# Kernel tuning notes

Measured on AMD Instinct MI355X. Metric: run time of the kernel, lower is better.

The kernel has to match this reference:

```python
import jax, jax.numpy as jnp
import numpy as np

B, T, C, H, E, L = 4, 1024, 768, 12, 4, 2
DH = C // H


def setup_inputs() -> dict:
    key = jax.random.key(0)
    ks = jax.random.split(key, 10)
    s = 0.02  # init scale; keeps unscaled-attention logits sane (source has no 1/sqrt(d))
    w = lambda k, shape: (jax.random.normal(k, shape, jnp.float32) * s)
    z = lambda shape: jnp.zeros(shape, jnp.float32)
    return dict(
        x=jax.random.normal(ks[0], (B, T, C), jnp.float32),
        gate_W=w(ks[1], (C, E)), gate_b=z((E,)),
        Wq=w(ks[2], (E, L, C, C)), bq=z((E, L, C)),
        Wk=w(ks[3], (E, L, C, C)), bk=z((E, L, C)),
        Wv=w(ks[4], (E, L, C, C)), bv=z((E, L, C)),
        Wo=w(ks[5], (E, L, C, C)), bo=z((E, L, C)),
        ln_g=jnp.ones((E, L, C), jnp.float32), ln_b=z((E, L, C)),
        Wfc=w(ks[6], (E, L, C, 4 * C)), bfc=z((E, L, 4 * C)),
        Wpr=w(ks[7], (E, L, 4 * C, C)), bpr=z((E, L, C)),
    )


def _attn(x, Wq, bq, Wk, bk, Wv, bv, Wo, bo):
    # FlashAttention3 blockwise loop == exact full softmax(Q K^T) V, NO scaling, NO mask
    q = (x @ Wq + bq).reshape(B, T, H, DH)
    k = (x @ Wk + bk).reshape(B, T, H, DH)
    v = (x @ Wv + bv).reshape(B, T, H, DH)
    s = jnp.einsum('bqhd,bkhd->bhqk', q, k)
    p = jax.nn.softmax(s, axis=-1)
    o = jnp.einsum('bhqk,bkhd->bqhd', p, v).reshape(B, T, C)
    return o @ Wo + bo


def _ln(x, g, b, eps=1e-5):
    m = x.mean(-1, keepdims=True)
    v = ((x - m) ** 2).mean(-1, keepdims=True)
    return (x - m) * jax.lax.rsqrt(v + eps) * g + b


def _expert(x, Wq, bq, Wk, bk, Wv, bv, Wo, bo, ln_g, ln_b, Wfc, bfc, Wpr, bpr):
    # Sequential(attn, layernorm, mlp) x L — no residuals, dropout=0 (eval)
    for l in range(L):
        x = _attn(x, Wq[l], bq[l], Wk[l], bk[l], Wv[l], bv[l], Wo[l], bo[l])
        x = _ln(x, ln_g[l], ln_b[l])
        h = jax.nn.gelu(x @ Wfc[l] + bfc[l], approximate=True)  # tanh GELU
        x = h @ Wpr[l] + bpr[l]
    return x


def reference(x, gate_W, gate_b, Wq, bq, Wk, bk, Wv, bv, Wo, bo,
              ln_g, ln_b, Wfc, bfc, Wpr, bpr):
    gate_probs = jax.nn.softmax(x @ gate_W + gate_b, axis=-1)  # [B,T,E]
    expert_fn = jax.vmap(_expert, in_axes=(None,) + (0,) * 14)
    eo = expert_fn(x, Wq, bq, Wk, bk, Wv, bv, Wo, bo, ln_g, ln_b, Wfc, bfc, Wpr, bpr)  # [E,B,T,C]
    return jnp.einsum('bte,ebtc->btc', gate_probs, eo)
```

## Files before the change

### kernel.cpp

```cpp
#include <hip/hip_runtime.h>

#define B_ 4
#define T_ 1024
#define C_ 768
#define H_ 12
#define E_ 4
#define L_ 2
#define DH_ 64
#define M_ (B_*T_)
#define QKVS_ (3*C_)
#define LOG2E_ 1.4426950408889634f

typedef __attribute__((ext_vector_type(8))) short bf16x8;
typedef __attribute__((ext_vector_type(4))) float f32x4;

__device__ __forceinline__ unsigned short f2bf(float f) {
  unsigned int u = __float_as_uint(f);
  unsigned int r = (u + 0x7FFFu + ((u >> 16) & 1u)) >> 16;
  return (unsigned short)r;
}
__device__ __forceinline__ float bf2f(unsigned short s) {
  return __uint_as_float(((unsigned int)s) << 16);
}
__device__ __forceinline__ unsigned int cvt_pk_bf16(float lo, float hi) {
  unsigned int r;
  asm("v_cvt_pk_bf16_f32 %0, %1, %2" : "=v"(r) : "v"(lo), "v"(hi));
  return r;
}

typedef __attribute__((address_space(1))) unsigned int gu32;
typedef __attribute__((address_space(3))) unsigned int lu32;
__device__ __forceinline__ void gld_lds16(const void* g, void* l) {
  __builtin_amdgcn_global_load_lds((gu32*)g, (lu32*)l, 16, 0, 0);
}

__device__ __forceinline__ float gelu_fast(float x) {
  float u = 0.7978845608028654f * x * (1.0f + 0.044715f * x * x);
  float d = 1.0f + exp2f(-2.8853900817779268f * u);
  return x * __builtin_amdgcn_rcpf(d);
}

template <int ACT>
__global__ __launch_bounds__(512, 2) void gemm256(
    const unsigned short* __restrict__ A, const unsigned short* __restrict__ Bt,
    const float* __restrict__ bias, unsigned short* __restrict__ D,
    int M, int N, int K, long long sA, long long sB, long long sBias, long long sD,
    float bscale)
{
  __shared__ unsigned short shA[4][256*32];
  __shared__ unsigned short shB[4][256*32];
  const int tid = threadIdx.x;
  const int lane = tid & 63, wid = tid >> 6;
  const int l15 = lane & 15, lhi = lane >> 4;
  const int wm = wid >> 2, wn = wid & 3;

  const int gx = gridDim.x, gxy = gx * gridDim.y;
  const int nwg = gxy * gridDim.z;
  int flat = blockIdx.z*gxy + blockIdx.y*gx + blockIdx.x;
  flat = (flat & 7) * (nwg >> 3) + (flat >> 3);
  const int g = flat / gxy;
  const int rem = flat - g*gxy;
  const int by = rem / gx, bx = rem - by*gx;
  const int m0 = by * 256, n0 = bx * 256;

  const unsigned short* Ab = A + (size_t)g * sA;
  const unsigned short* Bb = Bt + (size_t)g * sB;
  const float* biasb = bias + (size_t)g * sBias;
  unsigned short* Db = D + (size_t)g * sD;

  f32x4 acc[8][4] = {};

  const int l15h = l15 >> 1;
  const int s8 = (((((l15 & 1) << 2) | lhi) ^ (l15h & 7)) << 3);
  const int arp = wm*64;
  const int brp = wn*32;

  auto stageA = [&](int slot, int kh) {
    const int kb = kh << 5;
    #pragma unroll
    for (int iss = 0; iss < 2; ++iss) {
      const int c = tid + iss*512;
      const int q = c >> 3, pp = (c & 7) ^ (q & 7);
      gld_lds16(Ab + (size_t)(m0 + (q << 1) + (pp >> 2))*K + kb + ((pp & 3) << 3),
                &shA[slot][c*8]);
    }
  };
  auto stageB = [&](int slot, int kh) {
    const int kb = kh << 5;
    #pragma unroll
    for (int iss = 0; iss < 2; ++iss) {
      const int c = tid + iss*512;
      const int q = c >> 3, pp = (c & 7) ^ (q & 7);
      gld_lds16(Bb + (size_t)(n0 + (q << 1) + (pp >> 2))*K + kb + ((pp & 3) << 3),
                &shB[slot][c*8]);
    }
  };

  auto phase = [&](int slot, int mh, int stSel, int stSlot, int stKh, int vmN) {
    bf16x8 afr[4], bfr[4];
    #pragma unroll
    for (int i = 0; i < 4; ++i)
      afr[i] = *(const bf16x8*)&shA[slot][(arp + mh*32 + i*8 + l15h)*64 + s8];
    #pragma unroll
    for (int nf = 0; nf < 4; ++nf)
      bfr[nf] = *(const bf16x8*)&shB[slot][(brp + nf*8 + l15h)*64 + s8];
    if (stSel == 1) stageA(stSlot, stKh);
    else if (stSel == 2) stageB(stSlot, stKh);
    if (vmN == 4) asm volatile("s_waitcnt vmcnt(4)" ::: "memory");
    else if (vmN == 0) asm volatile("s_waitcnt vmcnt(0)" ::: "memory");
    __builtin_amdgcn_s_barrier();
    __builtin_amdgcn_s_setprio(1);
    #pragma unroll
    for (int i = 0; i < 4; ++i)
      #pragma unroll
      for (int nf = 0; nf < 4; ++nf)
        acc[mh*4+i][nf] = __builtin_amdgcn_mfma_f32_16x16x32_bf16(
            afr[i], bfr[nf], acc[mh*4+i][nf], 0, 0, 0);
    __builtin_amdgcn_s_setprio(0);
    __builtin_amdgcn_s_barrier();
  };

  const int nkt = K >> 6;
  const int nkh = nkt << 1;

  stageA(0, 0); stageB(0, 0);
  stageA(1, 1); stageB(1, 1);
  stageA(2, 2); stageB(2, 2);
  asm volatile("s_waitcnt vmcnt(4)" ::: "memory");
  __builtin_amdgcn_s_barrier();

  for (int k = 0; k < nkt; ++k) {
    const int s0 = (2*k) & 3, s1 = s0 + 1;
    const int m3 = 2*k + 3, m4 = 2*k + 4;
    const bool f3 = m3 < nkh, f4 = m4 < nkh;
    phase(s0, 0, f3 ? 1 : 0, m3 & 3, m3, -1);
    phase(s0, 1, f3 ? 2 : 0, m3 & 3, m3, -1);
    phase(s1, 0, f4 ? 1 : 0, m4 & 3, m4, -1);
    phase(s1, 1, f4 ? 2 : 0, m4 & 3, m4, f4 ? 4 : (f3 ? 0 : -1));
  }

  unsigned short* cbuf = (unsigned short*)&shA[0][0];
  const int lr = tid >> 4, ckk = tid & 15;
  const int growb = m0 + ((lr >> 4) ? 128 : 0) + (lr & 15);
  #pragma unroll
  for (int mf = 0; mf < 8; ++mf) {
    __builtin_amdgcn_s_barrier();
    #pragma unroll
    for (int nf = 0; nf < 4; ++nf) {
      const int col = wn*64 + nf*16 + l15;
      const float bv = bscale * biasb[n0 + col];
      #pragma unroll
      for (int r = 0; r < 4; ++r) {
        float v = acc[mf][nf][r] + bv;
        if (ACT == 1) v = gelu_fast(v);
        cbuf[(wm*16 + lhi*4 + r)*264 + col] = f2bf(v);
      }
    }
    __builtin_amdgcn_s_barrier();
    const size_t growN = (size_t)(growb + mf*16) * N + n0;
    #pragma unroll
    for (int cc2 = 0; cc2 < 2; ++cc2) {
      const int c = ckk + cc2*16;
      uint4 v = *(const uint4*)&cbuf[lr*264 + c*8];
      *(uint4*)&Db[growN + c*8] = v;
    }
  }
}

__global__ __launch_bounds__(256) void flash_attn(
    const unsigned short* __restrict__ qkv, const unsigned short* __restrict__ vt,
    unsigned short* __restrict__ o)
{
  __shared__ unsigned short shK[2][64*64];
  __shared__ unsigned short shV[2][64*64];
  __shared__ unsigned short shP[4][16*64];
  const int tid = threadIdx.x;
  const int wid = tid >> 6, lane = tid & 63;
  const int l15 = lane & 15, lhi = lane >> 4;
  const int qt = blockIdx.x, h = blockIdx.y, eb = blockIdx.z;

  const unsigned short* qrow = qkv + ((size_t)eb*T_ + qt*64 + wid*16 + l15) * QKVS_ + h*DH_;
  bf16x8 aq0 = *(const bf16x8*)(qrow + lhi*8);
  bf16x8 aq1 = *(const bf16x8*)(qrow + 32 + lhi*8);

  f32x4 oacc[4] = {};
  float lpart = 0.f;

  const int krow = tid >> 3;
  const int swzsrc = (((tid & 7) ^ (krow & 7)) << 3);
  const unsigned short* kbase = qkv + (size_t)eb*T_*QKVS_ + C_ + h*DH_;
  const unsigned short* vbase = vt + ((size_t)eb*H_ + h)*DH_*T_;

  auto stage = [&](int buf, int kt) {
    #pragma unroll
    for (int p = 0; p < 2; ++p) {
      gld_lds16(kbase + (size_t)(kt*64 + krow + p*32)*QKVS_ + swzsrc,
                &shK[buf][(p*256 + wid*64)*8]);
      gld_lds16(vbase + (size_t)(krow + p*32)*T_ + kt*64 + swzsrc,
                &shV[buf][(p*256 + wid*64)*8]);
    }
  };

  stage(0, 0);
  __syncthreads();
  int cur = 0;
  const int swzr = l15 & 7;
  const int c0 = (lhi ^ swzr) << 3;
  const int c1 = ((4 + lhi) ^ swzr) << 3;
  const int pwbase = l15*64 + ((lhi & 1) << 2);
  const int pwh = lhi >> 1;

  for (int kt = 0; kt < T_/64; ++kt) {
    if (kt + 1 < T_/64) stage(cur ^ 1, kt + 1);

    f32x4 s[4];
    #pragma unroll
    for (int kb = 0; kb < 4; ++kb) {
      const int row = (kb*16 + l15)*64;
      bf16x8 bk0 = *(const bf16x8*)&shK[cur][row + c0];
      bf16x8 bk1 = *(const bf16x8*)&shK[cur][row + c1];
      f32x4 z = {};
      z = __builtin_amdgcn_mfma_f32_16x16x32_bf16(bk0, aq0, z, 0, 0, 0);
      s[kb] = __builtin_amdgcn_mfma_f32_16x16x32_bf16(bk1, aq1, z, 0, 0, 0);
    }
    unsigned int pk0[4], pk1[4];
    #pragma unroll
    for (int kb = 0; kb < 4; ++kb) {
      #pragma unroll
      for (int r = 0; r < 4; ++r) {
        float pv = exp2f(s[kb][r]);
        s[kb][r] = pv;
        lpart += pv;
      }
      pk0[kb] = cvt_pk_bf16(s[kb][0], s[kb][1]);
      pk1[kb] = cvt_pk_bf16(s[kb][2], s[kb][3]);
    }
    #pragma unroll
    for (int kb = 0; kb < 4; ++kb) {
      const int chunk = (2*kb + pwh) ^ swzr;
      uint2 w = {pk0[kb], pk1[kb]};
      *(uint2*)&shP[wid][pwbase + chunk*8] = w;
    }
    bf16x8 pa0 = *(const bf16x8*)&shP[wid][l15*64 + c0];
    bf16x8 pa1 = *(const bf16x8*)&shP[wid][l15*64 + c1];
    #pragma unroll
    for (int n = 0; n < 4; ++n) {
      const int row = (n*16 + l15)*64;
      bf16x8 bv0 = *(const bf16x8*)&shV[cur][row + c0];
      bf16x8 bv1 = *(const bf16x8*)&shV[cur][row + c1];
      oacc[n] = __builtin_amdgcn_mfma_f32_16x16x32_bf16(pa0, bv0, oacc[n], 0, 0, 0);
      oacc[n] = __builtin_amdgcn_mfma_f32_16x16x32_bf16(pa1, bv1, oacc[n], 0, 0, 0);
    }
    __syncthreads();
    cur ^= 1;
  }
  lpart += __shfl_xor(lpart, 16);
  lpart += __shfl_xor(lpart, 32);
  float li[4];
  #pragma unroll
  for (int r = 0; r < 4; ++r) li[r] = __shfl(lpart, lhi*4 + r);
  #pragma unroll
  for (int n = 0; n < 4; ++n)
    #pragma unroll
    for (int r = 0; r < 4; ++r) {
      float v = oacc[n][r] / li[r];
      o[((size_t)eb*T_ + qt*64 + wid*16 + lhi*4 + r) * C_ + h*DH_ + n*16 + l15] = f2bf(v);
    }
}

__global__ void transpose_cast(const float* __restrict__ in, unsigned short* __restrict__ out,
                               int K, int N, long long inStride, long long outStride, float scale)
{
  __shared__ float tile[32][33];
  const float* src = in + (size_t)blockIdx.z * inStride;
  unsigned short* dst = out + (size_t)blockIdx.z * outStride;
  const int tx = threadIdx.x, ty = threadIdx.y;
  const int k0 = blockIdx.y*32, n0 = blockIdx.x*32;
  #pragma unroll
  for (int j = 0; j < 32; j += 8)
    tile[ty+j][tx] = src[(size_t)(k0+ty+j)*N + n0+tx];
  __syncthreads();
  #pragma unroll
  for (int j = 0; j < 32; j += 8)
    dst[(size_t)(n0+ty+j)*K + k0+tx] = f2bf(scale * tile[tx][ty+j]);
}

__global__ __launch_bounds__(256) void build_qkv_bias(
    const float* __restrict__ bq, const float* __restrict__ bk, const float* __restrict__ bv,
    float* __restrict__ dst, int l)
{
  const int i = blockIdx.x*256 + threadIdx.x;
  const int g = i / C_, c = i - g*C_;
  const size_t src = ((size_t)g*L_ + l)*C_ + c;
  dst[(size_t)g*QKVS_ + c]        = LOG2E_ * bq[src];
  dst[(size_t)g*QKVS_ + C_ + c]   = bk[src];
  dst[(size_t)g*QKVS_ + 2*C_ + c] = bv[src];
}

__global__ void transpose_v_kernel(const unsigned short* __restrict__ qkv, unsigned short* __restrict__ vt)
{
  __shared__ unsigned short tile[32][33];
  const int t0 = blockIdx.x * 32, d0 = blockIdx.y * 32;
  const int z = blockIdx.z;
  const int h = z % H_, eb = z / H_;
  const int tx = threadIdx.x, ty = threadIdx.y;
  #pragma unroll
  for (int j = 0; j < 32; j += 8)
    tile[ty+j][tx] = qkv[((size_t)eb*T_ + t0+ty+j)*QKVS_ + 2*C_ + h*DH_ + d0 + tx];
  __syncthreads();
  #pragma unroll
  for (int j = 0; j < 32; j += 8)
    vt[((size_t)z*DH_ + d0+ty+j)*T_ + t0 + tx] = tile[tx][ty+j];
}

__global__ __launch_bounds__(256) void ln_kernel(
    const unsigned short* __restrict__ in, unsigned short* __restrict__ out,
    const float* __restrict__ g, const float* __restrict__ b)
{
  const int row = blockIdx.x * 4 + (threadIdx.x >> 6);
  const int lane = threadIdx.x & 63;
  const int e = row >> 12;
  const unsigned short* ir = in + (size_t)row * C_;
  unsigned short* orow = out + (size_t)row * C_;
  const float* gg = g + (size_t)e * (L_*C_);
  const float* bb = b + (size_t)e * (L_*C_);
  float v[12]; float s = 0.f, s2 = 0.f;
  #pragma unroll
  for (int j = 0; j < 12; ++j) {
    float x = bf2f(ir[lane + 64*j]);
    v[j] = x; s += x; s2 += x*x;
  }
  #pragma unroll
  for (int d = 32; d; d >>= 1) { s += __shfl_xor(s, d); s2 += __shfl_xor(s2, d); }
  float mean = s * (1.f/C_);
  float var = s2 * (1.f/C_) - mean*mean;
  float rstd = rsqrtf(var + 1e-5f);
  #pragma unroll
  for (int j = 0; j < 12; ++j) {
    int c = lane + 64*j;
    orow[c] = f2bf((v[j]-mean)*rstd*gg[c] + bb[c]);
  }
}

__global__ __launch_bounds__(256) void gate_kernel(
    const float* __restrict__ x, const float* __restrict__ gw, const float* __restrict__ gb,
    float* __restrict__ gp)
{
  const int row = blockIdx.x * 4 + (threadIdx.x >> 6);
  const int lane = threadIdx.x & 63;
  const float* xr = x + (size_t)row * C_;
  float a0=0.f, a1=0.f, a2=0.f, a3=0.f;
  for (int i = lane; i < C_; i += 64) {
    float xv = xr[i];
    float4 w = ((const float4*)gw)[i];
    a0 += xv*w.x; a1 += xv*w.y; a2 += xv*w.z; a3 += xv*w.w;
  }
  #pragma unroll
  for (int d = 32; d; d >>= 1) {
    a0 += __shfl_xor(a0,d); a1 += __shfl_xor(a1,d);
    a2 += __shfl_xor(a2,d); a3 += __shfl_xor(a3,d);
  }
  if (lane == 0) {
    a0 += gb[0]; a1 += gb[1]; a2 += gb[2]; a3 += gb[3];
    float m = fmaxf(fmaxf(a0,a1), fmaxf(a2,a3));
    float e0 = __expf(a0-m), e1 = __expf(a1-m), e2 = __expf(a2-m), e3 = __expf(a3-m);
    float inv = 1.f/(e0+e1+e2+e3);
    float4 r = {e0*inv, e1*inv, e2*inv, e3*inv};
    ((float4*)gp)[row] = r;
  }
}

__global__ __launch_bounds__(256) void cast_x_kernel(const float* __restrict__ x,
                                                     unsigned short* __restrict__ xbf)
{
  const size_t i = (size_t)blockIdx.x * 256 + threadIdx.x;
  float4 v = ((const float4*)x)[i];
  ushort4 u;
  u.x = f2bf(v.x); u.y = f2bf(v.y); u.z = f2bf(v.z); u.w = f2bf(v.w);
  #pragma unroll
  for (int e = 0; e < E_; ++e)
    ((ushort4*)(xbf + (size_t)e * ((size_t)M_*C_)))[i] = u;
}

__global__ __launch_bounds__(256) void combine_kernel(
    const unsigned short* __restrict__ xbf, const float* __restrict__ gp, float* __restrict__ out)
{
  const size_t i = (size_t)blockIdx.x * 256 + threadIdx.x;
  const int row = (int)((i*4) / C_);
  float4 gpv = ((const float4*)gp)[row];
  const float* gpf = (const float*)&gpv;
  float r0=0.f, r1=0.f, r2=0.f, r3=0.f;
  #pragma unroll
  for (int e = 0; e < E_; ++e) {
    ushort4 u = ((const ushort4*)(xbf + (size_t)e*((size_t)M_*C_)))[i];
    float ge = gpf[e];
    r0 += ge*bf2f(u.x); r1 += ge*bf2f(u.y); r2 += ge*bf2f(u.z); r3 += ge*bf2f(u.w);
  }
  float4 res = {r0, r1, r2, r3};
  ((float4*)out)[i] = res;
}

extern "C" void kernel_launch(void* const* d_in, const int* in_sizes, int n_in,
                              void* d_out, int out_size, void* d_ws, size_t ws_size,
                              hipStream_t stream) {
  const float* x      = (const float*)d_in[0];
  const float* gate_W = (const float*)d_in[1];
  const float* gate_b = (const float*)d_in[2];
  const float* Wq = (const float*)d_in[3];
  const float* bq = (const float*)d_in[4];
  const float* Wk = (const float*)d_in[5];
  const float* bk = (const float*)d_in[6];
  const float* Wv = (const float*)d_in[7];
  const float* bv = (const float*)d_in[8];
  const float* Wo = (const float*)d_in[9];
  const float* bo = (const float*)d_in[10];
  const float* ln_g = (const float*)d_in[11];
  const float* ln_b = (const float*)d_in[12];
  const float* Wfc = (const float*)d_in[13];
  const float* bfc = (const float*)d_in[14];
  const float* Wpr = (const float*)d_in[15];
  const float* bpr = (const float*)d_in[16];
  float* out = (float*)d_out;

  const size_t CC  = (size_t)C_*C_;
  const size_t C4C = (size_t)C_*4*C_;
  const size_t MC  = (size_t)M_*C_;
  const size_t M4C = (size_t)M_*4*C_;

  char* p = (char*)d_ws;
  auto carve = [&](size_t bytes) { char* r = p; p += (bytes + 255) & ~(size_t)255; return r; };
  unsigned short* wqkvT = (unsigned short*)carve(E_*3*CC*2);
  unsigned short* woT   = (unsigned short*)carve(E_*CC*2);
  unsigned short* wfcT  = (unsigned short*)carve(E_*C4C*2);
  unsigned short* wprT  = (unsigned short*)carve(E_*C4C*2);
  unsigned short* xbf   = (unsigned short*)carve(E_*MC*2);
  unsigned short* r1    = (unsigned short*)carve((size_t)4*E_*MC*2);
  float* gp   = (float*)carve((size_t)M_*E_*4);
  float* bqkv = (float*)carve((size_t)E_*QKVS_*4);

  unsigned short* qkvb = r1;
  unsigned short* vtb  = r1 + (size_t)3*E_*MC;
  unsigned short* ob   = xbf;
  unsigned short* tb   = vtb;
  unsigned short* hb   = r1;

  dim3 blk256(256);
  dim3 blk512(512);
  dim3 blkT(32, 8);

  cast_x_kernel<<<dim3((unsigned)(MC/4/256)), blk256, 0, stream>>>(x, xbf);
  gate_kernel<<<dim3(M_/4), blk256, 0, stream>>>(x, gate_W, gate_b, gp);

  for (int l = 0; l < L_; ++l) {
    transpose_cast<<<dim3(24,24,E_), blkT, 0, stream>>>(Wq + l*CC, wqkvT,          C_, C_, (long long)(L_*CC), (long long)(3*CC), LOG2E_);
    transpose_cast<<<dim3(24,24,E_), blkT, 0, stream>>>(Wk + l*CC, wqkvT + CC,     C_, C_, (long long)(L_*CC), (long long)(3*CC), 1.0f);
    transpose_cast<<<dim3(24,24,E_), blkT, 0, stream>>>(Wv + l*CC, wqkvT + 2*CC,   C_, C_, (long long)(L_*CC), (long long)(3*CC), 1.0f);
    transpose_cast<<<dim3(24,24,E_), blkT, 0, stream>>>(Wo + l*CC,  woT,  C_,   C_,   (long long)(L_*CC),  (long long)CC, 1.0f);
    transpose_cast<<<dim3(96,24,E_), blkT, 0, stream>>>(Wfc + l*C4C, wfcT, C_,   4*C_, (long long)(L_*C4C), (long long)C4C, 1.0f);
    transpose_cast<<<dim3(24,96,E_), blkT, 0, stream>>>(Wpr + l*C4C, wprT, 4*C_, C_,   (long long)(L_*C4C), (long long)C4C, 1.0f);
    build_qkv_bias<<<dim3(E_*C_/256), blk256, 0, stream>>>(bq, bk, bv, bqkv, l);

    gemm256<0><<<dim3(QKVS_/256, M_/256, E_), blk512, 0, stream>>>(
        xbf, wqkvT, bqkv, qkvb, M_, QKVS_, C_, (long long)MC, (long long)(3*CC), (long long)QKVS_, (long long)M_*QKVS_, 1.0f);

    transpose_v_kernel<<<dim3(T_/32, DH_/32, E_*B_*H_), blkT, 0, stream>>>(qkvb, vtb);
    flash_attn<<<dim3(T_/64, H_, E_*B_), blk256, 0, stream>>>(qkvb, vtb, ob);

    gemm256<0><<<dim3(C_/256, M_/256, E_), blk512, 0, stream>>>(
        ob, woT, bo + l*C_, tb, M_, C_, C_, (long long)MC, (long long)CC, (long long)(L_*C_), (long long)MC, 1.0f);

    ln_kernel<<<dim3(E_*M_/4), blk256, 0, stream>>>(tb, xbf, ln_g + l*C_, ln_b + l*C_);

    gemm256<1><<<dim3(4*C_/256, M_/256, E_), blk512, 0, stream>>>(
        xbf, wfcT, bfc + l*4*C_, hb, M_, 4*C_, C_, (long long)MC, (long long)C4C, (long long)(L_*4*C_), (long long)M4C, 1.0f);
    gemm256<0><<<dim3(C_/256, M_/256, E_), blk512, 0, stream>>>(
        hb, wprT, bpr + l*C_, xbf, M_, C_, 4*C_, (long long)M4C, (long long)C4C, (long long)(L_*C_), (long long)MC, 1.0f);
  }

  combine_kernel<<<dim3((unsigned)(MC/4/256)), blk256, 0, stream>>>(xbf, gp, out);
}
```

Baseline: 994.4 us.

## Restructure GEMM main loop to one barrier per k-half with deeper prefetch

Replaces the four-phase-per-k-tile GEMM loop, which had two barriers per phase, with a single loop over 32-wide k-halves. Each iteration loads all A and B fragments, issues the A and B staging for three steps ahead, runs both MFMA halves, then does a single waitcnt plus barrier. The aim is to cut barrier and synchronization overhead and let more global loads stay in flight. The cost is higher register pressure from holding eight A fragments, and more outstanding VMEM counters to track.

Result: faster. 962.8 us (-3.2%).

```diff
diff --git a/kernel.cpp b/kernel.cpp
--- a/kernel.cpp
+++ b/kernel.cpp
@@ -96,47 +96,50 @@
     }
   };
 
-  auto phase = [&](int slot, int mh, int stSel, int stSlot, int stKh, int vmN) {
-    bf16x8 afr[4], bfr[4];
-    #pragma unroll
-    for (int i = 0; i < 4; ++i)
-      afr[i] = *(const bf16x8*)&shA[slot][(arp + mh*32 + i*8 + l15h)*64 + s8];
+  const int nkt = K >> 6;
+  const int nkh = nkt << 1;
+
+  stageA(0, 0); stageB(0, 0);
+  stageA(1, 1); stageB(1, 1);
+  stageA(2, 2); stageB(2, 2);
+  asm volatile("s_waitcnt vmcnt(8)" ::: "memory");
+  __builtin_amdgcn_s_barrier();
+
+  for (int m = 0; m < nkh; ++m) {
+    const int slot = m & 3;
+    bf16x8 bfr[4], af0[4], af1[4];
     #pragma unroll
     for (int nf = 0; nf < 4; ++nf)
       bfr[nf] = *(const bf16x8*)&shB[slot][(brp + nf*8 + l15h)*64 + s8];
-    if (stSel == 1) stageA(stSlot, stKh);
-    else if (stSel == 2) stageB(stSlot, stKh);
-    if (vmN == 4) asm volatile("s_waitcnt vmcnt(4)" ::: "memory");
-    else if (vmN == 0) asm volatile("s_waitcnt vmcnt(0)" ::: "memory");
-    __builtin_amdgcn_s_barrier();
+    #pragma unroll
+    for (int i = 0; i < 4; ++i)
+      af0[i] = *(const bf16x8*)&shA[slot][(arp + i*8 + l15h)*64 + s8];
+    #pragma unroll
+    for (int i = 0; i < 4; ++i)
+      af1[i] = *(const bf16x8*)&shA[slot][(arp + 32 + i*8 + l15h)*64 + s8];
+    const int mst = m + 3;
+    if (mst < nkh) { stageA(mst & 3, mst); stageB(mst & 3, mst); }
     __builtin_amdgcn_s_setprio(1);
     #pragma unroll
     for (int i = 0; i < 4; ++i)
       #pragma unroll
       for (int nf = 0; nf < 4; ++nf)
-        acc[mh*4+i][nf] = __builtin_amdgcn_mfma_f32_16x16x32_bf16(
-            afr[i], bfr[nf], acc[mh*4+i][nf], 0, 0, 0);
+        acc[i][nf] = __builtin_amdgcn_mfma_f32_16x16x32_bf16(
+            af0[i], bfr[nf], acc[i][nf], 0, 0, 0);
+    #pragma unroll
+    for (int i = 0; i < 4; ++i)
+      #pragma unroll
+      for (int nf = 0; nf < 4; ++nf)
+        acc[4+i][nf] = __builtin_amdgcn_mfma_f32_16x16x32_bf16(
+            af1[i], bfr[nf], acc[4+i][nf], 0, 0, 0);
     __builtin_amdgcn_s_setprio(0);
-    __builtin_amdgcn_s_barrier();
-  };
-
-  const int nkt = K >> 6;
-  const int nkh = nkt << 1;
-
-  stageA(0, 0); stageB(0, 0);
-  stageA(1, 1); stageB(1, 1);
-  stageA(2, 2); stageB(2, 2);
-  asm volatile("s_waitcnt vmcnt(4)" ::: "memory");
-  __builtin_amdgcn_s_barrier();
-
-  for (int k = 0; k < nkt; ++k) {
-    const int s0 = (2*k) & 3, s1 = s0 + 1;
-    const int m3 = 2*k + 3, m4 = 2*k + 4;
-    const bool f3 = m3 < nkh, f4 = m4 < nkh;
-    phase(s0, 0, f3 ? 1 : 0, m3 & 3, m3, -1);
-    phase(s0, 1, f3 ? 2 : 0, m3 & 3, m3, -1);
-    phase(s1, 0, f4 ? 1 : 0, m4 & 3, m4, -1);
-    phase(s1, 1, f4 ? 2 : 0, m4 & 3, m4, f4 ? 4 : (f3 ? 0 : -1));
+    if (m + 1 < nkh) {
+      const int nout = 4*((m+2 < nkh) + (m+3 < nkh));
+      if (nout == 8)      asm volatile("s_waitcnt vmcnt(8)" ::: "memory");
+      else if (nout == 4) asm volatile("s_waitcnt vmcnt(4)" ::: "memory");
+      else                asm volatile("s_waitcnt vmcnt(0)" ::: "memory");
+      __builtin_amdgcn_s_barrier();
+    }
   }
 
   unsigned short* cbuf = (unsigned short*)&shA[0][0];
```
